# Performance work log

Measured on AMD Instinct MI355X. Metric: run time of the kernel, lower is better.

## Reference

```python
import jax, jax.numpy as jnp
import numpy as np

NUM_HEADS = 16
CAPACITY = 512
ROPE_BASE = 10000.0

def _rope_factor(positions, dim):
    # freqs = exp(linspace(0,-1,dim//2) * log(base)), shape (dim//2,)
    freqs = jnp.exp(jnp.linspace(0.0, -1.0, dim // 2) * jnp.log(jnp.float32(ROPE_BASE)))
    angles = positions[..., None] * freqs            # (..., seq, dim//2)
    return jnp.concatenate([jnp.sin(angles), jnp.cos(angles)], axis=-1)  # (..., seq, dim)

def setup_inputs() -> dict:
    key = jax.random.key(0)
    ks = jax.random.split(key, 6)
    B, Sq, Skv, D = 4, 4096, 4096, 1024
    return {
        "query_seq": jax.random.normal(ks[0], (B, Sq, D), jnp.float32),
        "value_seq": jax.random.normal(ks[1], (B, Skv, D), jnp.float32),
        "router_w": jax.random.normal(ks[2], (1, D), jnp.float32) * 0.02,
        "q_w": jax.random.normal(ks[3], (D, D), jnp.float32) * 0.02,
        "kv_w": jax.random.normal(ks[4], (2 * D, D), jnp.float32) * 0.02,
        "out_w": jax.random.normal(ks[5], (D, D), jnp.float32) * 0.02,
    }

def reference(query_seq, value_seq, router_w, q_w, kv_w, out_w):
    B, Sq, D = query_seq.shape
    Skv = value_seq.shape[1]
    H, C = NUM_HEADS, CAPACITY
    d = D // H

    # router + top-k capacity selection over the sequence dim
    rw = jnp.einsum("bsd,od->bs", query_seq, router_w).astype(jnp.float32)  # (B,Sq)
    top_w, top_idx = jax.lax.top_k(rw, C)                                   # (B,C)

    # gather selected queries
    resampled = jnp.take_along_axis(query_seq, top_idx[:, :, None], axis=1)  # (B,C,D)

    q = jnp.einsum("bcd,ed->bce", resampled, q_w)        # (B,C,H*d)
    kv = jnp.einsum("bsd,ed->bse", value_seq, kv_w)      # (B,Skv,2*H*d)
    k, v = jnp.split(kv, 2, axis=-1)

    q = q.reshape(B, C, H, d).transpose(0, 2, 1, 3)      # (B,H,C,d)
    k = k.reshape(B, Skv, H, d).transpose(0, 2, 1, 3)    # (B,H,Skv,d)
    v = v.reshape(B, Skv, H, d).transpose(0, 2, 1, 3)

    # RoPE-style elementwise modulation (faithful to source: x * cat(sin, cos))
    q_pos = top_idx.astype(jnp.float32)[:, None, :]      # (B,1,C)
    q = q * _rope_factor(q_pos, d)                       # (B,H,C,d)
    k_pos = jnp.arange(Skv, dtype=jnp.float32)[None, :]  # (1,Skv)
    k = k * _rope_factor(k_pos, d)[None]                 # broadcast over (B,H)

    # SDPA
    scores = jnp.einsum("bhcd,bhsd->bhcs", q, k) / jnp.sqrt(jnp.float32(d))
    att = jnp.einsum("bhcs,bhsd->bhcd", jax.nn.softmax(scores, axis=-1), v)

    att = att.transpose(0, 2, 1, 3).reshape(B, C, H * d)  # (B,C,D)
    att = jnp.einsum("bce,de->bcd", att, out_w)           # (B,C,D)

    # weighted scatter back to full sequence
    src = att * top_w[:, :, None]
    out = jnp.zeros_like(query_seq).at[jnp.arange(B)[:, None], top_idx].set(src)
    return out
```

## Files before the change

kernel.cpp:

```cpp
#include <hip/hip_runtime.h>
#include <hip/hip_bf16.h>

#define B_  4
#define SQ  4096
#define SKV 4096
#define DM  1024
#define NH  16
#define HD  64
#define CAP 512

#define ASPLIT 4
#define KVPER  (SKV / ASPLIT)
#define AITERS (KVPER / 64)

typedef __attribute__((ext_vector_type(8))) short    short8;
typedef __attribute__((ext_vector_type(8))) __bf16   bf16v8;
typedef __attribute__((ext_vector_type(4))) float    f32x4;
typedef __attribute__((ext_vector_type(4))) unsigned short ushort4v;
typedef __attribute__((ext_vector_type(4))) unsigned int   uint4v;

static __device__ __forceinline__ unsigned short f2bf(float f) {
    unsigned u = __float_as_uint(f);
    u += 0x7FFFu + ((u >> 16) & 1u);
    return (unsigned short)(u >> 16);
}

static __device__ __forceinline__ f32x4 mfma_bf16(short8 a, short8 b, f32x4 c) {
    return __builtin_amdgcn_mfma_f32_16x16x32_bf16(
        __builtin_bit_cast(bf16v8, a), __builtin_bit_cast(bf16v8, b), c, 0, 0, 0);
}

#define GLD16(gp, lp)                                                              \
    __builtin_amdgcn_global_load_lds(                                              \
        (__attribute__((address_space(1))) void*)(gp),                             \
        (__attribute__((address_space(3))) void*)(lp), 16, 0, 0)

__global__ void __launch_bounds__(256) k_convert(const float* __restrict__ in,
                                                 unsigned short* __restrict__ out) {
    size_t i = (size_t)blockIdx.x * 256 + threadIdx.x;
    float4 f = ((const float4*)in)[i];
    ushort4v o = { f2bf(f.x), f2bf(f.y), f2bf(f.z), f2bf(f.w) };
    ((ushort4v*)out)[i] = o;
}

__global__ void __launch_bounds__(256) k_rope(float* __restrict__ tab) {
    int g = blockIdx.x * 256 + threadIdx.x;
    int pos = g >> 6, i = g & 63, j = i & 31;
    float freq = expf(-(float)j * (logf(10000.0f) / 31.0f));
    float ang  = (float)pos * freq;
    tab[g] = (i < 32) ? sinf(ang) : cosf(ang);
}

__global__ void __launch_bounds__(256) k_router(const float* __restrict__ q,
                                                const float* __restrict__ wv,
                                                float* __restrict__ rw) {
    int row  = blockIdx.x * 4 + (threadIdx.x >> 6);
    int lane = threadIdx.x & 63;
    const float* p  = q  + (size_t)row * DM + lane * 16;
    const float* wp = wv + lane * 16;
    float s = 0.f;
#pragma unroll
    for (int j = 0; j < 4; j++) {
        float4 a = ((const float4*)p)[j];
        float4 b = ((const float4*)wp)[j];
        s += a.x * b.x + a.y * b.y + a.z * b.z + a.w * b.w;
    }
#pragma unroll
    for (int m = 32; m > 0; m >>= 1) s += __shfl_xor(s, m, 64);
    if (lane == 0) rw[row] = s;
}

__global__ void __launch_bounds__(1024) k_topk(const float* __restrict__ rw,
                                               int* __restrict__ sel,
                                               float* __restrict__ selw) {
    __shared__ unsigned long long keys[4096];
    int b = blockIdx.x, t = threadIdx.x;
    for (int i = t; i < 4096; i += 1024) {
        float v = rw[b * 4096 + i];
        unsigned u = __float_as_uint(v);
        u = (u & 0x80000000u) ? ~u : (u | 0x80000000u);
        keys[i] = ((unsigned long long)(~u) << 32) | (unsigned)i;
    }
    __syncthreads();
    for (int k = 2; k <= 4096; k <<= 1)
        for (int j = k >> 1; j > 0; j >>= 1) {
            for (int i = t; i < 4096; i += 1024) {
                int ixj = i ^ j;
                if (ixj > i) {
                    bool up = ((i & k) == 0);
                    unsigned long long a = keys[i], c = keys[ixj];
                    if ((a > c) == up) { keys[i] = c; keys[ixj] = a; }
                }
            }
            __syncthreads();
        }
    for (int i = t; i < 512; i += 1024) {
        unsigned idx = (unsigned)(keys[i] & 0xFFFFFFFFu);
        sel[b * 512 + i]  = (int)idx;
        selw[b * 512 + i] = rw[b * 4096 + idx];
    }
}

__global__ void __launch_bounds__(256) k_gather(const float* __restrict__ q,
                                                const int* __restrict__ sel,
                                                unsigned short* __restrict__ out) {
    int row = blockIdx.x;
    int b = row >> 9;
    int s = sel[row];
    const float4* src = (const float4*)(q + ((size_t)b * SQ + s) * DM);
    ushort4v* dst = (ushort4v*)(out + (size_t)row * DM);
    float4 f = src[threadIdx.x];
    ushort4v o = { f2bf(f.x), f2bf(f.y), f2bf(f.z), f2bf(f.w) };
    dst[threadIdx.x] = o;
}

__global__ void __launch_bounds__(256) k_gemm_kv(
    const unsigned short* __restrict__ A,
    const unsigned short* __restrict__ Bw,
    const float* __restrict__ rope_tab,
    unsigned short* __restrict__ ok,
    unsigned short* __restrict__ ov) {
    __shared__ unsigned short lA [2][128 * 32];
    __shared__ unsigned short lBk[2][128 * 32];
    __shared__ unsigned short lBv[2][128 * 32];
    const int tid = threadIdx.x;
    const int w = tid >> 6, lane = tid & 63, quad = lane >> 4, l16 = lane & 15;
    const int wr = w >> 1, wc = w & 1;
    const int bid0 = blockIdx.y * 8 + blockIdx.x;
    const int bid  = (bid0 & 7) * 128 + (bid0 >> 3);
    const int mBase = (bid >> 3) << 7;
    const int nBase = (bid & 7) << 7;

    f32x4 accK[4][4] = {};
    f32x4 accV[4][4] = {};

    auto stage = [&](int buf, int k0) {
#pragma unroll
        for (int is = 0; is < 2; is++) {
            int slot = is * 256 + tid;
            int row = slot >> 2, sc2 = slot & 3;
            int kc = (sc2 - (row >> 1)) & 3;
            size_t koff = (size_t)k0 + kc * 8;
            const char* ga = (const char*)A  + (((size_t)(mBase + row) * DM) + koff) * 2;
            GLD16(ga, (char*)&lA[buf][0] + slot * 16);
            const char* gk = (const char*)Bw + (((size_t)(nBase + row) * DM) + koff) * 2;
            GLD16(gk, (char*)&lBk[buf][0] + slot * 16);
            const char* gv = (const char*)Bw + (((size_t)(nBase + 1024 + row) * DM) + koff) * 2;
            GLD16(gv, (char*)&lBv[buf][0] + slot * 16);
        }
    };

    stage(0, 0);
    __syncthreads();

    for (int t = 0; t < DM / 32; t++) {
        if (t + 1 < DM / 32) stage((t + 1) & 1, (t + 1) << 5);
        const unsigned short* bA = &lA [t & 1][0];
        const unsigned short* bK = &lBk[t & 1][0];
        const unsigned short* bV = &lBv[t & 1][0];
        short8 af[4], bk[4], bv[4];
#pragma unroll
        for (int tt = 0; tt < 4; tt++) {
            int rA = wr * 64 + tt * 16 + l16;
            af[tt] = *(const short8*)&bA[rA * 32 + (((quad + (rA >> 1)) & 3) * 8)];
            int rB = wc * 64 + tt * 16 + l16;
            bk[tt] = *(const short8*)&bK[rB * 32 + (((quad + (rB >> 1)) & 3) * 8)];
            bv[tt] = *(const short8*)&bV[rB * 32 + (((quad + (rB >> 1)) & 3) * 8)];
        }
#pragma unroll
        for (int tm = 0; tm < 4; tm++)
#pragma unroll
            for (int tn = 0; tn < 4; tn++) {
                accK[tm][tn] = mfma_bf16(af[tm], bk[tn], accK[tm][tn]);
                accV[tm][tn] = mfma_bf16(bv[tn], af[tm], accV[tm][tn]);
            }
        __syncthreads();
    }

#pragma unroll
    for (int tm = 0; tm < 4; tm++)
#pragma unroll
        for (int tn = 0; tn < 4; tn++)
#pragma unroll
            for (int r = 0; r < 4; r++) {
                {
                    float v = accK[tm][tn][r];
                    int m = mBase + wr * 64 + tm * 16 + quad * 4 + r;
                    int n = nBase + wc * 64 + tn * 16 + l16;
                    int b = m >> 12, s = m & 4095;
                    int h = n >> 6, i = n & 63;
                    v *= rope_tab[(s << 6) | i];
                    ok[(((size_t)(b * NH + h) * SKV) + s) * HD + i] = f2bf(v);
                }
                {
                    float v = accV[tm][tn][r];
                    int e = nBase + wc * 64 + tn * 16 + quad * 4 + r;
                    int m = mBase + wr * 64 + tm * 16 + l16;
                    int h = e >> 6, i = e & 63;
                    int b = m >> 12, s = m & 4095;
                    ov[(((size_t)(b * NH + h) * HD) + i) * SKV + s] = f2bf(v);
                }
            }
}

template <int MODE, int BN>
__global__ void __launch_bounds__(256) k_gemm(
    const unsigned short* __restrict__ A,
    const unsigned short* __restrict__ Bw,
    int M, int N, int K,
    const float* __restrict__ rope_tab,
    const int* __restrict__ sel,
    const float* __restrict__ selw,
    unsigned short* __restrict__ obf,
    float* __restrict__ of) {
    constexpr int TN = BN / 32;
    constexpr int GX = DM / BN;
    __shared__ unsigned short lA[2][128 * 32];
    __shared__ unsigned short lB[2][BN * 32];
    const int tid = threadIdx.x;
    const int w = tid >> 6, lane = tid & 63, quad = lane >> 4, l16 = lane & 15;
    const int wr = w >> 1, wc = w & 1;
    const int nwg = GX * (M >> 7);
    const int bid0 = blockIdx.y * GX + blockIdx.x;
    const int bid  = (bid0 & 7) * (nwg >> 3) + (bid0 >> 3);
    const int mBase = (bid / GX) << 7;
    const int nBase = (bid % GX) * BN;

    f32x4 acc[4][TN] = {};

    auto stage = [&](int buf, int k0) {
#pragma unroll
        for (int is = 0; is < 2; is++) {
            int slot = is * 256 + tid;
            int row = slot >> 2, sc2 = slot & 3;
            int kc = (sc2 - (row >> 1)) & 3;
            const char* ga = (const char*)A + (((size_t)(mBase + row) * K) + k0 + kc * 8) * 2;
            GLD16(ga, (char*)&lA[buf][0] + slot * 16);
        }
#pragma unroll
        for (int is = 0; is < BN / 64; is++) {
            int slot = is * 256 + tid;
            int row = slot >> 2, sc2 = slot & 3;
            int kc = (sc2 - (row >> 1)) & 3;
            const char* gb = (const char*)Bw + (((size_t)(nBase + row) * K) + k0 + kc * 8) * 2;
            GLD16(gb, (char*)&lB[buf][0] + slot * 16);
        }
    };

    const int NT = K >> 5;
    stage(0, 0);
    __syncthreads();

    for (int t = 0; t < NT; t++) {
        if (t + 1 < NT) stage((t + 1) & 1, (t + 1) << 5);
        const unsigned short* bA = &lA[t & 1][0];
        const unsigned short* bB = &lB[t & 1][0];
        short8 af[4], bfr[TN];
#pragma unroll
        for (int tt = 0; tt < 4; tt++) {
            int r = wr * 64 + tt * 16 + l16;
            af[tt] = *(const short8*)&bA[r * 32 + (((quad + (r >> 1)) & 3) * 8)];
        }
#pragma unroll
        for (int tt = 0; tt < TN; tt++) {
            int r = wc * (BN / 2) + tt * 16 + l16;
            bfr[tt] = *(const short8*)&bB[r * 32 + (((quad + (r >> 1)) & 3) * 8)];
        }
#pragma unroll
        for (int tm = 0; tm < 4; tm++)
#pragma unroll
            for (int tn = 0; tn < TN; tn++)
                acc[tm][tn] = mfma_bf16(af[tm], bfr[tn], acc[tm][tn]);
        __syncthreads();
    }

#pragma unroll
    for (int tm = 0; tm < 4; tm++) {
#pragma unroll
        for (int tn = 0; tn < TN; tn++) {
#pragma unroll
            for (int r = 0; r < 4; r++) {
                float v = acc[tm][tn][r];
                int m = mBase + wr * 64 + tm * 16 + quad * 4 + r;
                int n = nBase + wc * (BN / 2) + tn * 16 + l16;
                if constexpr (MODE == 1) {
                    int b = m >> 9, c = m & 511;
                    int h = n >> 6, i = n & 63;
                    float rp = rope_tab[(sel[m] << 6) | i];
                    obf[(((size_t)(b * NH + h) * CAP) + c) * HD + i] =
                        f2bf(v * rp * 0.18033688011112042f);
                } else {
                    int b = m >> 9;
                    int s = sel[m];
                    of[(((size_t)b * SQ) + s) * DM + n] = v * selw[m];
                }
            }
        }
    }
}

template <int C>
static __device__ __forceinline__ void att_step(
    int it, int base, int sr, int sp, int quad, int l16,
    const unsigned short* __restrict__ kb, const unsigned short* __restrict__ vb,
    unsigned short (*lK)[64 * 72], unsigned short (*lV)[64 * 72],
    short8 (&rk)[2], short8 (&rv)[2],
    const short8 (&qf)[2][2],
    f32x4 (&o)[2][4], f32x4 (&lsum)[2], const short8 ones) {
    if (it + 1 < AITERS) {
        unsigned short* dK = &lK[C ^ 1][sr * 72 + sp * 16];
        unsigned short* dV = &lV[C ^ 1][sr * 72 + sp * 16];
        *(short8*)dK       = rk[0];
        *(short8*)(dK + 8) = rk[1];
        *(short8*)dV       = rv[0];
        *(short8*)(dV + 8) = rv[1];
    }
    if (it + 2 < AITERS) {
        int s0 = base + (it + 2) * 64;
        const short8* srck = (const short8*)(kb + (size_t)(s0 + sr) * HD + sp * 16);
        rk[0] = srck[0]; rk[1] = srck[1];
        const short8* srcv = (const short8*)(vb + (size_t)sr * SKV + s0 + sp * 16);
        rv[0] = srcv[0]; rv[1] = srcv[1];
    }

    f32x4 sc[2][4] = {};
    __builtin_amdgcn_s_setprio(1);
#pragma unroll
    for (int tn = 0; tn < 4; tn++) {
        short8 kf0 = *(const short8*)&lK[C][(tn * 16 + l16) * 72 + quad * 8];
        short8 kf1 = *(const short8*)&lK[C][(tn * 16 + l16) * 72 + 32 + quad * 8];
#pragma unroll
        for (int rt = 0; rt < 2; rt++) {
            sc[rt][tn] = mfma_bf16(kf0, qf[rt][0], sc[rt][tn]);
            sc[rt][tn] = mfma_bf16(kf1, qf[rt][1], sc[rt][tn]);
        }
    }
    __builtin_amdgcn_s_setprio(0);
#pragma unroll
    for (int rt = 0; rt < 2; rt++)
#pragma unroll
        for (int tn = 0; tn < 4; tn++)
#pragma unroll
            for (int r = 0; r < 4; r++)
                sc[rt][tn][r] = exp2f(sc[rt][tn][r]);

    short8 pa[2][2];
#pragma unroll
    for (int rt = 0; rt < 2; rt++)
#pragma unroll
        for (int kc = 0; kc < 2; kc++) {
            uint4v wv;
#pragma unroll
            for (int t = 0; t < 4; t++) {
                unsigned pk;
                asm("v_cvt_pk_bf16_f32 %0, %1, %2"
                    : "=v"(pk)
                    : "v"(sc[rt][kc * 2 + (t >> 1)][(t & 1) * 2]),
                      "v"(sc[rt][kc * 2 + (t >> 1)][(t & 1) * 2 + 1]));
                wv[t] = pk;
            }
            pa[rt][kc] = __builtin_bit_cast(short8, wv);
        }

    __builtin_amdgcn_s_setprio(1);
#pragma unroll
    for (int kc = 0; kc < 2; kc++) {
        lsum[0] = mfma_bf16(pa[0][kc], ones, lsum[0]);
        lsum[1] = mfma_bf16(pa[1][kc], ones, lsum[1]);
#pragma unroll
        for (int tn = 0; tn < 4; tn++) {
            const unsigned short* vrow = &lV[C][(size_t)(tn * 16 + l16) * 72];
            uint2 g0 = *(const uint2*)(vrow + kc * 32 + quad * 4);
            uint2 g1 = *(const uint2*)(vrow + kc * 32 + 16 + quad * 4);
            uint4v wv = { g0.x, g0.y, g1.x, g1.y };
            short8 vf = __builtin_bit_cast(short8, wv);
            o[0][tn] = mfma_bf16(pa[0][kc], vf, o[0][tn]);
            o[1][tn] = mfma_bf16(pa[1][kc], vf, o[1][tn]);
        }
    }
    __builtin_amdgcn_s_setprio(0);
    __syncthreads();
}

__global__ void __launch_bounds__(256) k_attention(
    const unsigned short* __restrict__ Q,
    const unsigned short* __restrict__ Kg,
    const unsigned short* __restrict__ Vt,
    float* __restrict__ Opart,
    float* __restrict__ Lpart) {
    __shared__ unsigned short lK[2][64 * 72];
    __shared__ unsigned short lV[2][64 * 72];
    const int bid0 = (blockIdx.z * 64 + blockIdx.y) * 4 + blockIdx.x;
    const int bid  = (bid0 & 7) * 128 + (bid0 >> 3);
    const int bx = bid & 3, bh = (bid >> 2) & 63, z = bid >> 8;
    const int tid = threadIdx.x, w = tid >> 6, lane = tid & 63;
    const int quad = lane >> 4, l16 = lane & 15;
    const int qb = bx * 128 + w * 32;
    const int base = z * KVPER;

    short8 qf[2][2];
#pragma unroll
    for (int rt = 0; rt < 2; rt++) {
        const unsigned short* qp = Q + ((size_t)bh * CAP + qb + rt * 16 + l16) * HD + quad * 8;
        qf[rt][0] = *(const short8*)qp;
        qf[rt][1] = *(const short8*)(qp + 32);
    }

    const unsigned short* kb = Kg + (size_t)bh * SKV * HD;
    const unsigned short* vb = Vt + (size_t)bh * HD * SKV;
    const int sr = tid >> 2, sp = tid & 3;

    f32x4 o[2][4] = {};
    f32x4 lsum[2] = {};
    short8 ones = (short8)0x3F80;

    short8 rk[2], rv[2];
    {
        const short8* srck = (const short8*)(kb + (size_t)(base + sr) * HD + sp * 16);
        rk[0] = srck[0]; rk[1] = srck[1];
        const short8* srcv = (const short8*)(vb + (size_t)sr * SKV + base + sp * 16);
        rv[0] = srcv[0]; rv[1] = srcv[1];
    }
    {
        unsigned short* dK = &lK[0][sr * 72 + sp * 16];
        unsigned short* dV = &lV[0][sr * 72 + sp * 16];
        *(short8*)dK       = rk[0];
        *(short8*)(dK + 8) = rk[1];
        *(short8*)dV       = rv[0];
        *(short8*)(dV + 8) = rv[1];
    }
    {
        int s0 = base + 64;
        const short8* srck = (const short8*)(kb + (size_t)(s0 + sr) * HD + sp * 16);
        rk[0] = srck[0]; rk[1] = srck[1];
        const short8* srcv = (const short8*)(vb + (size_t)sr * SKV + s0 + sp * 16);
        rv[0] = srcv[0]; rv[1] = srcv[1];
    }
    __syncthreads();

    for (int it = 0; it < AITERS; it += 2) {
        att_step<0>(it,     base, sr, sp, quad, l16, kb, vb, lK, lV, rk, rv, qf, o, lsum, ones);
        att_step<1>(it + 1, base, sr, sp, quad, l16, kb, vb, lK, lV, rk, rv, qf, o, lsum, ones);
    }

    float* Ob = Opart + (((size_t)(z * 64 + bh)) * CAP + qb) * HD;
#pragma unroll
    for (int rt = 0; rt < 2; rt++)
#pragma unroll
        for (int tn = 0; tn < 4; tn++)
#pragma unroll
            for (int r = 0; r < 4; r++)
                Ob[(size_t)(rt * 16 + quad * 4 + r) * HD + tn * 16 + l16] = o[rt][tn][r];
    if (l16 == 0) {
#pragma unroll
        for (int rt = 0; rt < 2; rt++)
#pragma unroll
            for (int r = 0; r < 4; r++)
                Lpart[((size_t)(z * 64 + bh)) * CAP + qb + rt * 16 + quad * 4 + r] = lsum[rt][r];
    }
}

__global__ void __launch_bounds__(256) k_combine(
    const float* __restrict__ Opart, const float* __restrict__ Lpart,
    unsigned short* __restrict__ att) {
    int g = blockIdx.x * 256 + threadIdx.x;
    int dall = g & 1023, c = (g >> 10) & 511, b = g >> 19;
    int h = dall >> 6, dd = dall & 63;
    int bh = b * NH + h;
    float os = 0.f, ls = 0.f;
#pragma unroll
    for (int p = 0; p < ASPLIT; p++) {
        os += Opart[(((size_t)(p * 64 + bh)) * CAP + c) * HD + dd];
        ls += Lpart[((size_t)(p * 64 + bh)) * CAP + c];
    }
    att[g] = f2bf(os / ls);
}

extern "C" void kernel_launch(void* const* d_in, const int* in_sizes, int n_in,
                              void* d_out, int out_size, void* d_ws, size_t ws_size,
                              hipStream_t stream) {
    const float* query    = (const float*)d_in[0];
    const float* value    = (const float*)d_in[1];
    const float* router_w = (const float*)d_in[2];
    const float* q_w      = (const float*)d_in[3];
    const float* kv_w     = (const float*)d_in[4];
    const float* out_w    = (const float*)d_in[5];
    float* out = (float*)d_out;

    char* p = (char*)d_ws;
    unsigned short* value_bf = (unsigned short*)p; p += (size_t)B_ * SKV * DM * 2;
    unsigned short* kvw_bf   = (unsigned short*)p; p += (size_t)2 * DM * DM * 2;
    unsigned short* qw_bf    = (unsigned short*)p; p += (size_t)DM * DM * 2;
    unsigned short* ow_bf    = (unsigned short*)p; p += (size_t)DM * DM * 2;
    unsigned short* res_bf   = (unsigned short*)p; p += (size_t)B_ * CAP * DM * 2;
    unsigned short* q_attn   = (unsigned short*)p; p += (size_t)B_ * CAP * DM * 2;
    unsigned short* kbuf     = (unsigned short*)p; p += (size_t)B_ * SKV * DM * 2;
    unsigned short* vbuf     = (unsigned short*)p; p += (size_t)B_ * SKV * DM * 2;
    unsigned short* att_bf   = (unsigned short*)p; p += (size_t)B_ * CAP * DM * 2;
    float* rope_tab = (float*)p; p += (size_t)SKV * HD * 4;
    float* rw       = (float*)p; p += (size_t)B_ * SQ * 4;
    int*   sel      = (int*)p;   p += (size_t)B_ * CAP * 4;
    float* selw     = (float*)p; p += (size_t)B_ * CAP * 4;
    float* Opart = (float*)value_bf;
    float* Lpart = (float*)res_bf;

    hipMemsetAsync(d_out, 0, (size_t)out_size * sizeof(float), stream);

    k_convert<<<B_ * SKV * DM / 1024, 256, 0, stream>>>(value, value_bf);
    k_convert<<<2 * DM * DM / 1024, 256, 0, stream>>>(kv_w, kvw_bf);
    k_convert<<<DM * DM / 1024, 256, 0, stream>>>(q_w, qw_bf);
    k_convert<<<DM * DM / 1024, 256, 0, stream>>>(out_w, ow_bf);
    k_rope<<<SKV * HD / 256, 256, 0, stream>>>(rope_tab);
    k_router<<<B_ * SQ / 4, 256, 0, stream>>>(query, router_w, rw);
    k_topk<<<B_, 1024, 0, stream>>>(rw, sel, selw);
    k_gather<<<B_ * CAP, 256, 0, stream>>>(query, sel, res_bf);

    k_gemm_kv<<<dim3(DM / 128, B_ * SKV / 128), 256, 0, stream>>>(
        value_bf, kvw_bf, rope_tab, kbuf, vbuf);
    k_gemm<1, 64><<<dim3(DM / 64, B_ * CAP / 128), 256, 0, stream>>>(
        res_bf, qw_bf, B_ * CAP, DM, DM, rope_tab, sel, nullptr,
        q_attn, nullptr);

    k_attention<<<dim3(CAP / 128, B_ * NH, ASPLIT), 256, 0, stream>>>(
        q_attn, kbuf, vbuf, Opart, Lpart);
    k_combine<<<B_ * CAP * DM / 256, 256, 0, stream>>>(Opart, Lpart, att_bf);

    k_gemm<2, 64><<<dim3(DM / 64, B_ * CAP / 128), 256, 0, stream>>>(
        att_bf, ow_bf, B_ * CAP, DM, DM, nullptr, sel, selw,
        nullptr, out);
}
```

Before: 442.3 us.

## Triple-buffer KV projection GEMM with explicit vmcnt waits and single barrier

Converts the K/V projection GEMM from a double-buffered LDS pipeline to a triple-buffered one. The loads for tile t+2 are issued while tile t is computed, and a partial s_waitcnt vmcnt plus one barrier per step replaces the two __syncthreads. The aim is to hide global-load latency and cut barrier stalls in the main loop. It raises LDS use per block by half, which may reduce occupancy. Correctness relies on hand-counted vmcnt values and on the buffer index matching the unrolled tail.

```diff
diff --git a/kernel.cpp b/kernel.cpp
--- a/kernel.cpp
+++ b/kernel.cpp
@@ -120,9 +120,9 @@
     const float* __restrict__ rope_tab,
     unsigned short* __restrict__ ok,
     unsigned short* __restrict__ ov) {
-    __shared__ unsigned short lA [2][128 * 32];
-    __shared__ unsigned short lBk[2][128 * 32];
-    __shared__ unsigned short lBv[2][128 * 32];
+    __shared__ unsigned short lA [3][128 * 32];
+    __shared__ unsigned short lBk[3][128 * 32];
+    __shared__ unsigned short lBv[3][128 * 32];
     const int tid = threadIdx.x;
     const int w = tid >> 6, lane = tid & 63, quad = lane >> 4, l16 = lane & 15;
     const int wr = w >> 1, wc = w & 1;
@@ -130,6 +130,7 @@
     const int bid  = (bid0 & 7) * 128 + (bid0 >> 3);
     const int mBase = (bid >> 3) << 7;
     const int nBase = (bid & 7) << 7;
+    constexpr int NT = DM / 32;
 
     f32x4 accK[4][4] = {};
     f32x4 accV[4][4] = {};
@@ -150,32 +151,44 @@
         }
     };
 
+#define KV_STEP(T, CUR)                                                               \
+    do {                                                                              \
+        if ((T) + 1 < NT) asm volatile("s_waitcnt vmcnt(6)" ::: "memory");            \
+        else              asm volatile("s_waitcnt vmcnt(0)" ::: "memory");            \
+        __builtin_amdgcn_s_barrier();                                                 \
+        __builtin_amdgcn_sched_barrier(0);                                            \
+        if ((T) + 2 < NT) stage(((CUR) + 2) % 3, ((T) + 2) << 5);                     \
+        const unsigned short* bA = &lA [(CUR)][0];                                    \
+        const unsigned short* bK = &lBk[(CUR)][0];                                    \
+        const unsigned short* bV = &lBv[(CUR)][0];                                    \
+        short8 af[4], bk[4], bv[4];                                                   \
+        _Pragma("unroll")                                                             \
+        for (int tt = 0; tt < 4; tt++) {                                              \
+            int rA = wr * 64 + tt * 16 + l16;                                         \
+            af[tt] = *(const short8*)&bA[rA * 32 + (((quad + (rA >> 1)) & 3) * 8)];   \
+            int rB = wc * 64 + tt * 16 + l16;                                         \
+            bk[tt] = *(const short8*)&bK[rB * 32 + (((quad + (rB >> 1)) & 3) * 8)];   \
+            bv[tt] = *(const short8*)&bV[rB * 32 + (((quad + (rB >> 1)) & 3) * 8)];   \
+        }                                                                             \
+        _Pragma("unroll")                                                             \
+        for (int tm = 0; tm < 4; tm++)                                                \
+            _Pragma("unroll")                                                         \
+            for (int tn = 0; tn < 4; tn++) {                                          \
+                accK[tm][tn] = mfma_bf16(af[tm], bk[tn], accK[tm][tn]);               \
+                accV[tm][tn] = mfma_bf16(bv[tn], af[tm], accV[tm][tn]);               \
+            }                                                                         \
+    } while (0)
+
     stage(0, 0);
-    __syncthreads();
-
-    for (int t = 0; t < DM / 32; t++) {
-        if (t + 1 < DM / 32) stage((t + 1) & 1, (t + 1) << 5);
-        const unsigned short* bA = &lA [t & 1][0];
-        const unsigned short* bK = &lBk[t & 1][0];
-        const unsigned short* bV = &lBv[t & 1][0];
-        short8 af[4], bk[4], bv[4];
-#pragma unroll
-        for (int tt = 0; tt < 4; tt++) {
-            int rA = wr * 64 + tt * 16 + l16;
-            af[tt] = *(const short8*)&bA[rA * 32 + (((quad + (rA >> 1)) & 3) * 8)];
-            int rB = wc * 64 + tt * 16 + l16;
-            bk[tt] = *(const short8*)&bK[rB * 32 + (((quad + (rB >> 1)) & 3) * 8)];
-            bv[tt] = *(const short8*)&bV[rB * 32 + (((quad + (rB >> 1)) & 3) * 8)];
-        }
-#pragma unroll
-        for (int tm = 0; tm < 4; tm++)
-#pragma unroll
-            for (int tn = 0; tn < 4; tn++) {
-                accK[tm][tn] = mfma_bf16(af[tm], bk[tn], accK[tm][tn]);
-                accV[tm][tn] = mfma_bf16(bv[tn], af[tm], accV[tm][tn]);
-            }
-        __syncthreads();
-    }
+    stage(1, 32);
+    for (int t = 0; t < NT - 2; t += 3) {
+        KV_STEP(t,     0);
+        KV_STEP(t + 1, 1);
+        KV_STEP(t + 2, 2);
+    }
+    KV_STEP(NT - 2, 0);
+    KV_STEP(NT - 1, 1);
+#undef KV_STEP
 
 #pragma unroll
     for (int tm = 0; tm < 4; tm++)
```

After: 469.3 us. 6.1% more time.

## Fuse prep kernels into one launch and replace bitonic top-k with rank counting

Applied to the files above, without the earlier changes.

Merges the output memset, the four fp32-to-bf16 conversions, the RoPE table build and the router dot product into one kernel that dispatches on block index, removing several launches and their serialization gaps. The single-block-per-batch bitonic sort for top-k becomes a parallel rank-count over 64 blocks, where each element counts how many values exceed it and writes itself if its rank is below capacity. This trades a log-squared sort with many barriers for O(N) comparisons per element. Ties are broken by index, so the output order should match the sort.

```diff
diff --git a/kernel.cpp b/kernel.cpp
--- a/kernel.cpp
+++ b/kernel.cpp
@@ -35,69 +35,86 @@
         (__attribute__((address_space(1))) void*)(gp),                             \
         (__attribute__((address_space(3))) void*)(lp), 16, 0, 0)
 
-__global__ void __launch_bounds__(256) k_convert(const float* __restrict__ in,
-                                                 unsigned short* __restrict__ out) {
-    size_t i = (size_t)blockIdx.x * 256 + threadIdx.x;
-    float4 f = ((const float4*)in)[i];
-    ushort4v o = { f2bf(f.x), f2bf(f.y), f2bf(f.z), f2bf(f.w) };
-    ((ushort4v*)out)[i] = o;
-}
-
-__global__ void __launch_bounds__(256) k_rope(float* __restrict__ tab) {
-    int g = blockIdx.x * 256 + threadIdx.x;
-    int pos = g >> 6, i = g & 63, j = i & 31;
-    float freq = expf(-(float)j * (logf(10000.0f) / 31.0f));
-    float ang  = (float)pos * freq;
-    tab[g] = (i < 32) ? sinf(ang) : cosf(ang);
-}
-
-__global__ void __launch_bounds__(256) k_router(const float* __restrict__ q,
-                                                const float* __restrict__ wv,
-                                                float* __restrict__ rw) {
-    int row  = blockIdx.x * 4 + (threadIdx.x >> 6);
-    int lane = threadIdx.x & 63;
-    const float* p  = q  + (size_t)row * DM + lane * 16;
-    const float* wp = wv + lane * 16;
-    float s = 0.f;
-#pragma unroll
-    for (int j = 0; j < 4; j++) {
-        float4 a = ((const float4*)p)[j];
-        float4 b = ((const float4*)wp)[j];
-        s += a.x * b.x + a.y * b.y + a.z * b.z + a.w * b.w;
-    }
-#pragma unroll
-    for (int m = 32; m > 0; m >>= 1) s += __shfl_xor(s, m, 64);
-    if (lane == 0) rw[row] = s;
-}
-
-__global__ void __launch_bounds__(1024) k_topk(const float* __restrict__ rw,
-                                               int* __restrict__ sel,
-                                               float* __restrict__ selw) {
-    __shared__ unsigned long long keys[4096];
-    int b = blockIdx.x, t = threadIdx.x;
-    for (int i = t; i < 4096; i += 1024) {
-        float v = rw[b * 4096 + i];
-        unsigned u = __float_as_uint(v);
-        u = (u & 0x80000000u) ? ~u : (u | 0x80000000u);
-        keys[i] = ((unsigned long long)(~u) << 32) | (unsigned)i;
-    }
+#define PREP_BLOCKS (16384 + 16384 + 2048 + 1024 + 1024 + 1024 + 4096)
+__global__ void __launch_bounds__(256) k_prep(
+    const float* __restrict__ value, const float* __restrict__ kv_w,
+    const float* __restrict__ q_w,   const float* __restrict__ out_w,
+    const float* __restrict__ query, const float* __restrict__ router_w,
+    float* __restrict__ out,
+    unsigned short* __restrict__ value_bf, unsigned short* __restrict__ kvw_bf,
+    unsigned short* __restrict__ qw_bf,    unsigned short* __restrict__ ow_bf,
+    float* __restrict__ rope_tab, float* __restrict__ rw) {
+    int bb = blockIdx.x;
+    const int tid = threadIdx.x;
+    if (bb < 16384) {
+        float4 z; z.x = z.y = z.z = z.w = 0.f;
+        ((float4*)out)[(size_t)bb * 256 + tid] = z;
+        return;
+    }
+    bb -= 16384;
+    if (bb < 16384 + 2048 + 1024 + 1024) {
+        const float* src; unsigned short* dst; int blk;
+        if (bb < 16384)                  { src = value; dst = value_bf; blk = bb; }
+        else if (bb < 16384 + 2048)      { src = kv_w;  dst = kvw_bf;  blk = bb - 16384; }
+        else if (bb < 16384 + 2048 + 1024) { src = q_w; dst = qw_bf;   blk = bb - (16384 + 2048); }
+        else                             { src = out_w; dst = ow_bf;   blk = bb - (16384 + 2048 + 1024); }
+        size_t i = (size_t)blk * 256 + tid;
+        float4 f = ((const float4*)src)[i];
+        ushort4v o = { f2bf(f.x), f2bf(f.y), f2bf(f.z), f2bf(f.w) };
+        ((ushort4v*)dst)[i] = o;
+        return;
+    }
+    bb -= 16384 + 2048 + 1024 + 1024;
+    if (bb < 1024) {
+        int g = bb * 256 + tid;
+        int pos = g >> 6, i = g & 63, j = i & 31;
+        float freq = expf(-(float)j * (logf(10000.0f) / 31.0f));
+        float ang  = (float)pos * freq;
+        rope_tab[g] = (i < 32) ? sinf(ang) : cosf(ang);
+        return;
+    }
+    bb -= 1024;
+    {
+        int row  = bb * 4 + (tid >> 6);
+        int lane = tid & 63;
+        const float* p  = query    + (size_t)row * DM + lane * 16;
+        const float* wp = router_w + lane * 16;
+        float s = 0.f;
+#pragma unroll
+        for (int j = 0; j < 4; j++) {
+            float4 a = ((const float4*)p)[j];
+            float4 b = ((const float4*)wp)[j];
+            s += a.x * b.x + a.y * b.y + a.z * b.z + a.w * b.w;
+        }
+#pragma unroll
+        for (int m = 32; m > 0; m >>= 1) s += __shfl_xor(s, m, 64);
+        if (lane == 0) rw[row] = s;
+    }
+}
+
+__global__ void __launch_bounds__(256) k_topk(const float* __restrict__ rw,
+                                              int* __restrict__ sel,
+                                              float* __restrict__ selw) {
+    __shared__ float vals[4096];
+    const int b = blockIdx.x >> 4;
+    const int blk = blockIdx.x & 15;
+    const int tid = threadIdx.x;
+    for (int i = tid; i < 4096; i += 256)
+        vals[i] = rw[b * 4096 + i];
     __syncthreads();
-    for (int k = 2; k <= 4096; k <<= 1)
-        for (int j = k >> 1; j > 0; j >>= 1) {
-            for (int i = t; i < 4096; i += 1024) {
-                int ixj = i ^ j;
-                if (ixj > i) {
-                    bool up = ((i & k) == 0);
-                    unsigned long long a = keys[i], c = keys[ixj];
-                    if ((a > c) == up) { keys[i] = c; keys[ixj] = a; }
-                }
-            }
-            __syncthreads();
-        }
-    for (int i = t; i < 512; i += 1024) {
-        unsigned idx = (unsigned)(keys[i] & 0xFFFFFFFFu);
-        sel[b * 512 + i]  = (int)idx;
-        selw[b * 512 + i] = rw[b * 4096 + idx];
+    const int e = blk * 256 + tid;
+    const float v = vals[e];
+    int rank = 0;
+#pragma unroll 4
+    for (int j = 0; j < 4096; j += 4) {
+        float4 u = *(const float4*)&vals[j];
+        rank += (u.x > v) + (u.y > v) + (u.z > v) + (u.w > v);
+        rank += (u.x == v && (j + 0) < e) + (u.y == v && (j + 1) < e)
+              + (u.z == v && (j + 2) < e) + (u.w == v && (j + 3) < e);
+    }
+    if (rank < 512) {
+        sel[b * 512 + rank]  = e;
+        selw[b * 512 + rank] = v;
     }
 }
 
@@ -504,15 +521,10 @@
     float* Opart = (float*)value_bf;
     float* Lpart = (float*)res_bf;
 
-    hipMemsetAsync(d_out, 0, (size_t)out_size * sizeof(float), stream);
-
-    k_convert<<<B_ * SKV * DM / 1024, 256, 0, stream>>>(value, value_bf);
-    k_convert<<<2 * DM * DM / 1024, 256, 0, stream>>>(kv_w, kvw_bf);
-    k_convert<<<DM * DM / 1024, 256, 0, stream>>>(q_w, qw_bf);
-    k_convert<<<DM * DM / 1024, 256, 0, stream>>>(out_w, ow_bf);
-    k_rope<<<SKV * HD / 256, 256, 0, stream>>>(rope_tab);
-    k_router<<<B_ * SQ / 4, 256, 0, stream>>>(query, router_w, rw);
-    k_topk<<<B_, 1024, 0, stream>>>(rw, sel, selw);
+    k_prep<<<PREP_BLOCKS, 256, 0, stream>>>(
+        value, kv_w, q_w, out_w, query, router_w,
+        out, value_bf, kvw_bf, qw_bf, ow_bf, rope_tab, rw);
+    k_topk<<<B_ * 16, 256, 0, stream>>>(rw, sel, selw);
     k_gather<<<B_ * CAP, 256, 0, stream>>>(query, sel, res_bf);
 
     k_gemm_kv<<<dim3(DM / 128, B_ * SKV / 128), 256, 0, stream>>>(
```

Measured after the change: 456.8 us. 3.3% more time.

## Replace bitonic top-k with parallel rank counting and halve attention KV split

Applied to the files above, without the earlier changes.

The single-block-per-batch bitonic sort for top-k selection is replaced by a rank-counting kernel spread across 16 blocks per batch. Each thread counts how many router scores beat its own and writes its index directly to that slot if it falls inside the capacity. This is meant to remove the many serialized sort passes and barriers on only four blocks. The attention split over the KV sequence also drops from 4 to 2, with the block swizzle adjusted to match. That means fewer partial results to combine, but also half as many attention blocks to fill the GPU.

```diff
diff --git a/kernel.cpp b/kernel.cpp
--- a/kernel.cpp
+++ b/kernel.cpp
@@ -9,7 +9,7 @@
 #define HD  64
 #define CAP 512
 
-#define ASPLIT 4
+#define ASPLIT 2
 #define KVPER  (SKV / ASPLIT)
 #define AITERS (KVPER / 64)
 
@@ -70,34 +70,29 @@
     if (lane == 0) rw[row] = s;
 }
 
-__global__ void __launch_bounds__(1024) k_topk(const float* __restrict__ rw,
-                                               int* __restrict__ sel,
-                                               float* __restrict__ selw) {
-    __shared__ unsigned long long keys[4096];
-    int b = blockIdx.x, t = threadIdx.x;
-    for (int i = t; i < 4096; i += 1024) {
-        float v = rw[b * 4096 + i];
-        unsigned u = __float_as_uint(v);
-        u = (u & 0x80000000u) ? ~u : (u | 0x80000000u);
-        keys[i] = ((unsigned long long)(~u) << 32) | (unsigned)i;
-    }
+__global__ void __launch_bounds__(256) k_topk(const float* __restrict__ rw,
+                                              int* __restrict__ sel,
+                                              float* __restrict__ selw) {
+    __shared__ float vals[4096];
+    const int b = blockIdx.x >> 4;
+    const int blk = blockIdx.x & 15;
+    const int tid = threadIdx.x;
+    for (int i = tid; i < 4096; i += 256)
+        vals[i] = rw[b * 4096 + i];
     __syncthreads();
-    for (int k = 2; k <= 4096; k <<= 1)
-        for (int j = k >> 1; j > 0; j >>= 1) {
-            for (int i = t; i < 4096; i += 1024) {
-                int ixj = i ^ j;
-                if (ixj > i) {
-                    bool up = ((i & k) == 0);
-                    unsigned long long a = keys[i], c = keys[ixj];
-                    if ((a > c) == up) { keys[i] = c; keys[ixj] = a; }
-                }
-            }
-            __syncthreads();
-        }
-    for (int i = t; i < 512; i += 1024) {
-        unsigned idx = (unsigned)(keys[i] & 0xFFFFFFFFu);
-        sel[b * 512 + i]  = (int)idx;
-        selw[b * 512 + i] = rw[b * 4096 + idx];
+    const int e = blk * 256 + tid;
+    const float v = vals[e];
+    int rank = 0;
+#pragma unroll 4
+    for (int j = 0; j < 4096; j += 4) {
+        float4 u = *(const float4*)&vals[j];
+        rank += (u.x > v) + (u.y > v) + (u.z > v) + (u.w > v);
+        rank += (u.x == v && (j + 0) < e) + (u.y == v && (j + 1) < e)
+              + (u.z == v && (j + 2) < e) + (u.w == v && (j + 3) < e);
+    }
+    if (rank < 512) {
+        sel[b * 512 + rank]  = e;
+        selw[b * 512 + rank] = v;
     }
 }
 
@@ -391,7 +386,7 @@
     __shared__ unsigned short lK[2][64 * 72];
     __shared__ unsigned short lV[2][64 * 72];
     const int bid0 = (blockIdx.z * 64 + blockIdx.y) * 4 + blockIdx.x;
-    const int bid  = (bid0 & 7) * 128 + (bid0 >> 3);
+    const int bid  = (bid0 & 7) * 64 + (bid0 >> 3);
     const int bx = bid & 3, bh = (bid >> 2) & 63, z = bid >> 8;
     const int tid = threadIdx.x, w = tid >> 6, lane = tid & 63;
     const int quad = lane >> 4, l16 = lane & 15;
@@ -512,7 +507,7 @@
     k_convert<<<DM * DM / 1024, 256, 0, stream>>>(out_w, ow_bf);
     k_rope<<<SKV * HD / 256, 256, 0, stream>>>(rope_tab);
     k_router<<<B_ * SQ / 4, 256, 0, stream>>>(query, router_w, rw);
-    k_topk<<<B_, 1024, 0, stream>>>(rw, sel, selw);
+    k_topk<<<B_ * 16, 256, 0, stream>>>(rw, sel, selw);
     k_gather<<<B_ * CAP, 256, 0, stream>>>(query, sel, res_bf);
 
     k_gemm_kv<<<dim3(DM / 128, B_ * SKV / 128), 256, 0, stream>>>(
```

After: 467.0 us. 1.06x slower.
